# Kernel optimization log

Hardware: AMD Instinct MI355X
Metric: run time of the kernel (lower is better)

Reference implementation:

```python
import jax, jax.numpy as jnp
import numpy as np

ROI = 400
HEADS = 4
DEPTH = 2
RATIO = 0.7
NUM_CLASSES = 2
DH = ROI // HEADS          # dim_head = 100
SCALE = DH ** -0.5
B = 64
HID = 2 * ROI              # ffn hidden = dim * 2


def setup_inputs() -> dict:
    key = jax.random.key(0)
    ks = jax.random.split(key, 24)
    s = 0.02

    def rn(k, shape, scale=s):
        return jax.random.normal(k, shape, dtype=jnp.float32) * scale

    inputs = jax.random.uniform(ks[0], (B, ROI, 2 * ROI), dtype=jnp.float32)
    return {
        "inputs": inputs,
        # structural feature selector (torch init: ones)
        "sc_sel": jnp.ones((ROI, ROI), jnp.float32),
        # attention (per layer, stacked): linears stored [in, out]
        "wq": rn(ks[1], (DEPTH, ROI, ROI)),
        "wk": rn(ks[2], (DEPTH, ROI, ROI)),
        "wv": rn(ks[3], (DEPTH, ROI, ROI)),
        "wo": rn(ks[4], (DEPTH, ROI, ROI)),
        "bo": jnp.zeros((DEPTH, ROI), jnp.float32),
        # feedforward
        "ffn_w1": rn(ks[5], (DEPTH, ROI, HID)),
        "ffn_b1": jnp.zeros((DEPTH, HID), jnp.float32),
        "ffn_w2": rn(ks[6], (DEPTH, HID, ROI)),
        "ffn_b2": jnp.zeros((DEPTH, ROI), jnp.float32),
        "ln_g": jnp.ones((DEPTH, ROI), jnp.float32),
        "ln_b": jnp.zeros((DEPTH, ROI), jnp.float32),
        # pooling (only layer 0's pooling is used since depth=2)
        "pool_ws": rn(ks[7], (ROI, 1), 1.0),
        "pool_wf": rn(ks[8], (ROI, 1), 1.0),
        "pmlp_w": rn(ks[9], (2, 1), 0.5),
        "pmlp_b": jnp.zeros((1,), jnp.float32),
        # readouts
        "r1w": rn(ks[10], (DEPTH, ROI, 128)),
        "r1b": jnp.zeros((DEPTH, 128), jnp.float32),
        "r2w": rn(ks[11], (DEPTH, 128, NUM_CLASSES)),
        "r2b": jnp.zeros((DEPTH, NUM_CLASSES), jnp.float32),
    }


def _layer_norm(x, g, b, eps=1e-5):
    mu = x.mean(-1, keepdims=True)
    var = ((x - mu) ** 2).mean(-1, keepdims=True)
    return (x - mu) * jax.lax.rsqrt(var + eps) * g + b


def _attention(x, m, wq, wk, wv, wo, bo):
    b, n, d = x.shape
    q = (x @ wq).reshape(b, n, HEADS, DH)
    k = (x @ wk).reshape(b, n, HEADS, DH)
    v = (x @ wv).reshape(b, n, HEADS, DH)
    dots = jnp.einsum("bihd,bjhd->bhij", q, k) * SCALE
    dots = dots * (1.0 + m[:, None])        # mask-modulated scores
    attn = jax.nn.softmax(dots, axis=-1)
    out = jnp.einsum("bhij,bjhd->bihd", attn, v).reshape(b, n, HEADS * DH)
    return out @ wo + bo


def _pool(x, m, pool_ws, pool_wf, pmlp_w, pmlp_b):
    b, n, d = x.shape
    k = int(RATIO * n)                       # static under jit
    s1 = jnp.sqrt(jnp.sum((m @ pool_ws[:n]) ** 2, axis=-1))   # [B, N]
    s2 = jnp.sqrt(jnp.sum((x @ pool_wf) ** 2, axis=-1))       # [B, N]
    S = jnp.stack([s1, s2], axis=-1)                          # [B, N, 2]
    scores = jax.nn.sigmoid((S @ pmlp_w + pmlp_b)).squeeze(-1)  # [B, N]
    _, idx = jax.lax.top_k(scores, k)
    idx = jnp.sort(idx, axis=-1)                              # [B, k]
    x_p = jnp.take_along_axis(x, idx[:, :, None], axis=1)     # [B, k, D]
    sw = jnp.take_along_axis(scores, idx, axis=1)[:, :, None]
    x_p = x_p * sw
    m_p = jax.vmap(lambda mb, ib: mb[ib[:, None], ib[None, :]])(m, idx)
    return x_p, m_p


def _forward(inputs, sc_sel, wq, wk, wv, wo, bo, ffn_w1, ffn_b1, ffn_w2,
             ffn_b2, ln_g, ln_b, pool_ws, pool_wf, pmlp_w, pmlp_b,
             r1w, r1b, r2w, r2b):
    fc = inputs[:, :, :ROI]
    sc = inputs[:, :, ROI:]
    sc = jnp.log10(sc + 1.0)
    mean = sc.mean(axis=(1, 2), keepdims=True)
    std = jnp.std(sc, axis=(1, 2), keepdims=True, ddof=1) + 1e-6
    sc = (sc - mean) / std
    M = sc * jax.nn.sigmoid(sc_sel)
    X = fc
    probs = []
    for i in range(DEPTH):
        X = _attention(X, M, wq[i], wk[i], wv[i], wo[i], bo[i]) + X
        h = jax.nn.gelu(X @ ffn_w1[i] + ffn_b1[i], approximate=False)
        h = h @ ffn_w2[i] + ffn_b2[i]
        X = _layer_norm(h + X, ln_g[i], ln_b[i])
        gf = X.mean(axis=1)
        logits = jax.nn.leaky_relu(gf @ r1w[i] + r1b[i], 0.01) @ r2w[i] + r2b[i]
        probs.append(jax.nn.softmax(logits, axis=-1))
        if i < DEPTH - 1:
            X, M = _pool(X, M, pool_ws, pool_wf, pmlp_w, pmlp_b)
    final_prob = jnp.stack(probs, axis=0).mean(axis=0)
    feat = X.mean(axis=1)
    feat = feat / jnp.maximum(jnp.linalg.norm(feat, axis=1, keepdims=True), 1e-12)
    return feat, final_prob


def reference(inputs, sc_sel, wq, wk, wv, wo, bo, ffn_w1, ffn_b1, ffn_w2,
              ffn_b2, ln_g, ln_b, pool_ws, pool_wf, pmlp_w, pmlp_b,
              r1w, r1b, r2w, r2b):
    return _forward(inputs, sc_sel, wq, wk, wv, wo, bo, ffn_w1, ffn_b1,
                    ffn_w2, ffn_b2, ln_g, ln_b, pool_ws, pool_wf, pmlp_w,
                    pmlp_b, r1w, r1b, r2w, r2b)
```

## Files before the change

kernel.cpp:

```cpp
#include <hip/hip_runtime.h>
#include <math.h>

#define ROI 400
#define HEADS 4
#define DH 100
#define NB 64
#define HIDF 800
#define NC 2
#define KPOOL 280
#define ATT_SCALE 0.1f
#define CTT 10

typedef __attribute__((ext_vector_type(8))) short short8v;
typedef __attribute__((ext_vector_type(8))) unsigned short u16x8;
typedef __attribute__((ext_vector_type(4))) float f32x4;

union U8 { short8v v; unsigned short u[8]; };

__device__ __forceinline__ unsigned short f2bf(float x) {
  unsigned int u = __float_as_uint(x);
  u += 0x7fffu + ((u >> 16) & 1u);
  return (unsigned short)(u >> 16);
}
__device__ __forceinline__ void split2(float x, unsigned short& h, unsigned short& l) {
  h = f2bf(x);
  float hf = __uint_as_float(((unsigned int)h) << 16);
  l = f2bf(x - hf);
}

__global__ __launch_bounds__(256) void pre_partial_kernel(const float* __restrict__ in,
                                                          double* __restrict__ pp) {
  int b = blockIdx.x, t = blockIdx.y;
  const float* p = in + (size_t)b * ROI * (2 * ROI);
  float s = 0.f, ss = 0.f;
  for (int e = threadIdx.x; e < 40 * ROI; e += 256) {
    int r = 40 * t + e / ROI, c = e % ROI;
    float v = log10f(p[(size_t)r * (2 * ROI) + ROI + c] + 1.0f);
    s += v; ss += v * v;
  }
  __shared__ double rs[256], rss[256];
  rs[threadIdx.x] = s; rss[threadIdx.x] = ss;
  __syncthreads();
  for (int st = 128; st > 0; st >>= 1) {
    if (threadIdx.x < st) { rs[threadIdx.x] += rs[threadIdx.x + st]; rss[threadIdx.x] += rss[threadIdx.x + st]; }
    __syncthreads();
  }
  if (threadIdx.x == 0) {
    pp[(b * CTT + t) * 2 + 0] = rs[0];
    pp[(b * CTT + t) * 2 + 1] = rss[0];
  }
}

__global__ __launch_bounds__(64) void pre_final_kernel(const double* __restrict__ pp,
                                                       float* __restrict__ meanb,
                                                       float* __restrict__ stdb) {
  int b = threadIdx.x;
  double s = 0.0, ss = 0.0;
  for (int t = 0; t < CTT; ++t) { s += pp[(b * CTT + t) * 2]; ss += pp[(b * CTT + t) * 2 + 1]; }
  const int n = ROI * ROI;
  double mean = s / n;
  double var = (ss - s * s / n) / (double)(n - 1);
  meanb[b] = (float)mean;
  stdb[b]  = (float)(sqrt(var) + 1e-6);
}

__global__ __launch_bounds__(256) void build_m_kernel(const float* __restrict__ in,
                                                      const float* __restrict__ sel,
                                                      const float* __restrict__ meanb,
                                                      const float* __restrict__ stdb,
                                                      float* __restrict__ M) {
  size_t e = (size_t)blockIdx.x * blockDim.x + threadIdx.x;
  const size_t total = (size_t)NB * ROI * ROI;
  if (e >= total) return;
  int c = (int)(e % ROI);
  int r = (int)((e / ROI) % ROI);
  int b = (int)(e / ((size_t)ROI * ROI));
  const float* row = in + ((size_t)b * ROI + r) * (2 * ROI);
  float v = log10f(row[ROI + c] + 1.0f);
  float sg = 1.0f / (1.0f + expf(-sel[r * ROI + c]));
  M[e] = ((v - meanb[b]) / stdb[b]) * sg;
}

struct PackDesc {
  const float* W;
  unsigned short* WH;
  unsigned short* WL;
  int K, N, nbx, blk0;
};
struct PackAll { PackDesc d[6]; };

__global__ __launch_bounds__(256) void packall_kernel(PackAll pa) {
  int gb = blockIdx.x;
  int i = 0;
#pragma unroll
  for (int j = 1; j < 6; ++j) if (gb >= pa.d[j].blk0) i = j;
  const float* __restrict__ W = pa.d[i].W;
  unsigned short* __restrict__ WH = pa.d[i].WH;
  unsigned short* __restrict__ WL = pa.d[i].WL;
  const int K = pa.d[i].K, N = pa.d[i].N;
  int lb = gb - pa.d[i].blk0;
  int bn = (lb % pa.d[i].nbx) * 64;
  int bk = (lb / pa.d[i].nbx) * 64;

  __shared__ float t[64][68];
  int r = threadIdx.x >> 2;
  int c0 = (threadIdx.x & 3) << 4;
  int gk = bk + r;
#pragma unroll
  for (int q = 0; q < 4; ++q) {
    int c = c0 + 4 * q;
    float4 v = make_float4(0.f, 0.f, 0.f, 0.f);
    if (gk < K && bn + c < N) v = *(const float4*)(W + (size_t)gk * N + bn + c);
    *(float4*)&t[r][c] = v;
  }
  __syncthreads();
  int gn = bn + r;
#pragma unroll
  for (int q = 0; q < 4; ++q) {
    int c = c0 + 4 * q;
    int gkk = bk + c;
    if (gn < N && gkk < K) {
      ushort4 h, l;
      split2(t[c + 0][r], h.x, l.x);
      split2(t[c + 1][r], h.y, l.y);
      split2(t[c + 2][r], h.z, l.z);
      split2(t[c + 3][r], h.w, l.w);
      *(ushort4*)(WH + (size_t)gn * K + gkk) = h;
      *(ushort4*)(WL + (size_t)gn * K + gkk) = l;
    }
  }
}

__global__ __launch_bounds__(256) void packa_kernel(const float* __restrict__ A, int lda, int K, int total4,
                                                    unsigned short* __restrict__ AH,
                                                    unsigned short* __restrict__ AL) {
  int e = blockIdx.x * 256 + threadIdx.x;
  if (e >= total4) return;
  int idx = e << 2;
  int row = idx / K, k = idx - row * K;
  float4 v = *(const float4*)(A + (size_t)row * lda + k);
  ushort4 h, l;
  split2(v.x, h.x, l.x); split2(v.y, h.y, l.y);
  split2(v.z, h.z, l.z); split2(v.w, h.w, l.w);
  *(ushort4*)(AH + (size_t)row * K + k) = h;
  *(ushort4*)(AL + (size_t)row * K + k) = l;
}

#define TBM 128
#define TBN 128
#define TBK 32
#define KP 40

template<int EPI>
__global__ __launch_bounds__(256) void mgemm_kernel(const unsigned short* __restrict__ AHp,
                                                    const unsigned short* __restrict__ ALp,
                                                    const unsigned short* __restrict__ WH,
                                                    const unsigned short* __restrict__ WL,
                                                    const float* __restrict__ bias,
                                                    const float* __restrict__ res, int ldr,
                                                    float* __restrict__ C,
                                                    unsigned short* __restrict__ CH,
                                                    unsigned short* __restrict__ CL,
                                                    int M, int N, int K) {
  __shared__ unsigned short Ah[TBM][KP], Al[TBM][KP], Bh[TBN][KP], Bl[TBN][KP];
  const int tid = threadIdx.x;
  const int lane = tid & 63;
  const int wid = tid >> 6;
  const int wm = wid >> 1, wn = wid & 1;
  const int l15 = lane & 15, l4 = lane >> 4;
  const int bm = blockIdx.y * TBM;
  const int bn = blockIdx.x * TBN;

  f32x4 acc[4][4];
#pragma unroll
  for (int i = 0; i < 4; ++i)
#pragma unroll
    for (int j = 0; j < 4; ++j) acc[i][j] = (f32x4){0.f, 0.f, 0.f, 0.f};

  for (int k0 = 0; k0 < K; k0 += TBK) {
#pragma unroll
    for (int it = 0; it < 2; ++it) {
      int c = tid + 256 * it;
      int row = c >> 2;
      int kq = (c & 3) << 3;
      u16x8 vh = {0, 0, 0, 0, 0, 0, 0, 0};
      u16x8 vl = {0, 0, 0, 0, 0, 0, 0, 0};
      if (k0 + kq + 8 <= K) {
        size_t off = (size_t)(bm + row) * K + k0 + kq;
        vh = *(const u16x8*)(AHp + off);
        vl = *(const u16x8*)(ALp + off);
      }
      *(u16x8*)&Ah[row][kq] = vh;
      *(u16x8*)&Al[row][kq] = vl;
    }
#pragma unroll
    for (int it = 0; it < 2; ++it) {
      int c = tid + 256 * it;
      int row = c >> 2;
      int kq = (c & 3) << 3;
      int gn = bn + row;
      u16x8 vh = {0, 0, 0, 0, 0, 0, 0, 0};
      u16x8 vl = {0, 0, 0, 0, 0, 0, 0, 0};
      if (gn < N && k0 + kq + 8 <= K) {
        size_t off = (size_t)gn * K + k0 + kq;
        vh = *(const u16x8*)(WH + off);
        vl = *(const u16x8*)(WL + off);
      }
      *(u16x8*)&Bh[row][kq] = vh;
      *(u16x8*)&Bl[row][kq] = vl;
    }
    __syncthreads();

    short8v ah[4], alo[4], bh[4], blo[4];
#pragma unroll
    for (int mf = 0; mf < 4; ++mf) {
      int r = wm * 64 + mf * 16 + l15;
      ah[mf]  = *(const short8v*)&Ah[r][l4 * 8];
      alo[mf] = *(const short8v*)&Al[r][l4 * 8];
    }
#pragma unroll
    for (int nf = 0; nf < 4; ++nf) {
      int r = wn * 64 + nf * 16 + l15;
      bh[nf]  = *(const short8v*)&Bh[r][l4 * 8];
      blo[nf] = *(const short8v*)&Bl[r][l4 * 8];
    }
#pragma unroll
    for (int mf = 0; mf < 4; ++mf)
#pragma unroll
      for (int nf = 0; nf < 4; ++nf) {
        acc[mf][nf] = __builtin_amdgcn_mfma_f32_16x16x32_bf16(ah[mf], bh[nf], acc[mf][nf], 0, 0, 0);
        acc[mf][nf] = __builtin_amdgcn_mfma_f32_16x16x32_bf16(ah[mf], blo[nf], acc[mf][nf], 0, 0, 0);
        acc[mf][nf] = __builtin_amdgcn_mfma_f32_16x16x32_bf16(alo[mf], bh[nf], acc[mf][nf], 0, 0, 0);
      }
    __syncthreads();
  }

#pragma unroll
  for (int mf = 0; mf < 4; ++mf) {
#pragma unroll
    for (int nf = 0; nf < 4; ++nf) {
      int col = bn + wn * 64 + nf * 16 + l15;
      if (col < N) {
        float bv = (EPI >= 1 && EPI != 6) ? bias[col] : 0.f;
        int row0 = bm + wm * 64 + mf * 16 + l4 * 4;
#pragma unroll
        for (int r = 0; r < 4; ++r) {
          float v = acc[mf][nf][r] + bv;
          int row = row0 + r;
          if (EPI == 2 || EPI == 5) v += res[(size_t)row * ldr + col];
          if (EPI == 4) {
            v = 0.5f * v * (1.0f + erff(v * 0.70710678118654752f));
            unsigned short hh, ll;
            split2(v, hh, ll);
            CH[(size_t)row * N + col] = hh;
            CL[(size_t)row * N + col] = ll;
          } else if (EPI == 5) {
            C[(size_t)row * N + col] = v;
            unsigned short hh, ll;
            split2(v, hh, ll);
            CH[(size_t)row * N + col] = hh;
            CL[(size_t)row * N + col] = ll;
          } else if (EPI == 6) {
            unsigned short hh, ll;
            split2(v, hh, ll);
            CH[(size_t)row * N + col] = hh;
            CL[(size_t)row * N + col] = ll;
          } else {
            C[(size_t)row * N + col] = v;
          }
        }
      }
    }
  }
}

#define FBJ 32

__global__ __launch_bounds__(256) void fattn_kernel(const unsigned short* __restrict__ QKVH,
                                                    const unsigned short* __restrict__ QKVL,
                                                    const float* __restrict__ Mm,
                                                    unsigned short* __restrict__ OH,
                                                    unsigned short* __restrict__ OL, int N) {
  const int ldq = 3 * ROI;
  __shared__ unsigned short Kh[FBJ][136], Kl[FBJ][136];
  __shared__ unsigned short Vth[112][40], Vtl[112][40];
  __shared__ unsigned short Ph[64][40], Pl[64][40];

  const int tid = threadIdx.x;
  const int lane = tid & 63;
  const int w = tid >> 6;
  const int l15 = lane & 15, l4 = lane >> 4;
  const int h = blockIdx.x & (HEADS - 1);
  const int b = blockIdx.x >> 2;
  const int i0 = blockIdx.y * 64;

  const float* Mb = Mm + (size_t)b * N * N;

  for (int e = tid; e < 12 * 40; e += 256) {
    Vth[100 + e / 40][e % 40] = 0; Vtl[100 + e / 40][e % 40] = 0;
  }

  int qr = i0 + 16 * w + l15; if (qr >= N) qr = N - 1;
  const unsigned short* qrH = QKVH + ((size_t)b * N + qr) * ldq + h * DH;
  const unsigned short* qrL = QKVL + ((size_t)b * N + qr) * ldq + h * DH;
  short8v qh[4], ql[4];
#pragma unroll
  for (int kg = 0; kg < 4; ++kg) {
    int d0v = kg * 32 + l4 * 8;
    U8 th, tl;
    if (d0v + 8 <= DH) {
      *(ushort4*)&th.u[0] = *(const ushort4*)(qrH + d0v);
      *(ushort4*)&th.u[4] = *(const ushort4*)(qrH + d0v + 4);
      *(ushort4*)&tl.u[0] = *(const ushort4*)(qrL + d0v);
      *(ushort4*)&tl.u[4] = *(const ushort4*)(qrL + d0v + 4);
    } else if (d0v < DH) {
      *(ushort4*)&th.u[0] = *(const ushort4*)(qrH + d0v);
      *(ushort4*)&tl.u[0] = *(const ushort4*)(qrL + d0v);
#pragma unroll
      for (int j = 4; j < 8; ++j) { th.u[j] = 0; tl.u[j] = 0; }
    } else {
#pragma unroll
      for (int j = 0; j < 8; ++j) { th.u[j] = 0; tl.u[j] = 0; }
    }
    qh[kg] = th.v; ql[kg] = tl.v;
  }

  float m_i[4], l_i[4];
  f32x4 o[7];
#pragma unroll
  for (int r = 0; r < 4; ++r) { m_i[r] = -INFINITY; l_i[r] = 0.f; }
#pragma unroll
  for (int ff = 0; ff < 7; ++ff) o[ff] = (f32x4){0.f, 0.f, 0.f, 0.f};

  const int njt = (N + FBJ - 1) / FBJ;
  for (int jt = 0; jt < njt; ++jt) {
    const int j0 = jt * FBJ;
    const int kv0 = j0 + l15, kv1 = j0 + l15 + 16;

    float mpre[4][2];
#pragma unroll
    for (int r = 0; r < 4; ++r) {
      int gq = i0 + 16 * w + l4 * 4 + r;
      int gqc = (gq < N) ? gq : N - 1;
      const float* Mr = Mb + (size_t)gqc * N;
      mpre[r][0] = (kv0 < N) ? Mr[kv0] : 0.f;
      mpre[r][1] = (kv1 < N) ? Mr[kv1] : 0.f;
    }

    __syncthreads();
    for (int e = tid; e < 32 * 32; e += 256) {
      int kv = e >> 5;
      int dq = (e & 31) << 2;
      int gj = j0 + kv; if (gj >= N) gj = N - 1;
      size_t off = ((size_t)b * N + gj) * ldq + ROI + h * DH + dq;
      ushort4 hh = {0, 0, 0, 0}, ll = {0, 0, 0, 0};
      if (dq < DH) { hh = *(const ushort4*)(QKVH + off); ll = *(const ushort4*)(QKVL + off); }
      *(ushort4*)&Kh[kv][dq] = hh;
      *(ushort4*)&Kl[kv][dq] = ll;
    }
    for (int e = tid; e < 400; e += 256) {
      int kvp = e & 15;
      int dq = (e >> 4) << 2;
      int gj0 = j0 + 2 * kvp;     if (gj0 >= N) gj0 = N - 1;
      int gj1 = j0 + 2 * kvp + 1; if (gj1 >= N) gj1 = N - 1;
      size_t o0 = ((size_t)b * N + gj0) * ldq + 2 * ROI + h * DH + dq;
      size_t o1 = ((size_t)b * N + gj1) * ldq + 2 * ROI + h * DH + dq;
      ushort4 aH = *(const ushort4*)(QKVH + o0);
      ushort4 bH = *(const ushort4*)(QKVH + o1);
      ushort4 aL = *(const ushort4*)(QKVL + o0);
      ushort4 bL = *(const ushort4*)(QKVL + o1);
      *(unsigned int*)&Vth[dq + 0][2 * kvp] = (unsigned int)aH.x | ((unsigned int)bH.x << 16);
      *(unsigned int*)&Vth[dq + 1][2 * kvp] = (unsigned int)aH.y | ((unsigned int)bH.y << 16);
      *(unsigned int*)&Vth[dq + 2][2 * kvp] = (unsigned int)aH.z | ((unsigned int)bH.z << 16);
      *(unsigned int*)&Vth[dq + 3][2 * kvp] = (unsigned int)aH.w | ((unsigned int)bH.w << 16);
      *(unsigned int*)&Vtl[dq + 0][2 * kvp] = (unsigned int)aL.x | ((unsigned int)bL.x << 16);
      *(unsigned int*)&Vtl[dq + 1][2 * kvp] = (unsigned int)aL.y | ((unsigned int)bL.y << 16);
      *(unsigned int*)&Vtl[dq + 2][2 * kvp] = (unsigned int)aL.z | ((unsigned int)bL.z << 16);
      *(unsigned int*)&Vtl[dq + 3][2 * kvp] = (unsigned int)aL.w | ((unsigned int)bL.w << 16);
    }
    __syncthreads();

    f32x4 sacc[2];
    sacc[0] = (f32x4){0.f, 0.f, 0.f, 0.f};
    sacc[1] = (f32x4){0.f, 0.f, 0.f, 0.f};
#pragma unroll
    for (int kg = 0; kg < 4; ++kg) {
#pragma unroll
      for (int f = 0; f < 2; ++f) {
        short8v bh = *(const short8v*)&Kh[l15 + 16 * f][kg * 32 + l4 * 8];
        short8v bl = *(const short8v*)&Kl[l15 + 16 * f][kg * 32 + l4 * 8];
        sacc[f] = __builtin_amdgcn_mfma_f32_16x16x32_bf16(qh[kg], bh, sacc[f], 0, 0, 0);
        sacc[f] = __builtin_amdgcn_mfma_f32_16x16x32_bf16(qh[kg], bl, sacc[f], 0, 0, 0);
        sacc[f] = __builtin_amdgcn_mfma_f32_16x16x32_bf16(ql[kg], bh, sacc[f], 0, 0, 0);
      }
    }

#pragma unroll
    for (int r = 0; r < 4; ++r) {
      float s0 = (kv0 < N) ? sacc[0][r] * ATT_SCALE * (1.0f + mpre[r][0]) : -INFINITY;
      float s1 = (kv1 < N) ? sacc[1][r] * ATT_SCALE * (1.0f + mpre[r][1]) : -INFINITY;
      float rm = fmaxf(s0, s1);
      rm = fmaxf(rm, __shfl_xor(rm, 1, 16));
      rm = fmaxf(rm, __shfl_xor(rm, 2, 16));
      rm = fmaxf(rm, __shfl_xor(rm, 4, 16));
      rm = fmaxf(rm, __shfl_xor(rm, 8, 16));
      float nm = fmaxf(m_i[r], rm);
      float fr = expf(m_i[r] - nm);
      float p0 = (kv0 < N) ? expf(s0 - nm) : 0.f;
      float p1 = (kv1 < N) ? expf(s1 - nm) : 0.f;
      float ts = p0 + p1;
      ts += __shfl_xor(ts, 1, 16);
      ts += __shfl_xor(ts, 2, 16);
      ts += __shfl_xor(ts, 4, 16);
      ts += __shfl_xor(ts, 8, 16);
      l_i[r] = l_i[r] * fr + ts;
      m_i[r] = nm;
#pragma unroll
      for (int ff = 0; ff < 7; ++ff) o[ff][r] *= fr;
      unsigned short h0, l0, h1, l1;
      split2(p0, h0, l0); split2(p1, h1, l1);
      int prow = 16 * w + l4 * 4 + r;
      Ph[prow][l15] = h0;      Pl[prow][l15] = l0;
      Ph[prow][l15 + 16] = h1; Pl[prow][l15 + 16] = l1;
    }
    __syncthreads();

    short8v ph = *(const short8v*)&Ph[16 * w + l15][l4 * 8];
    short8v pl = *(const short8v*)&Pl[16 * w + l15][l4 * 8];
#pragma unroll
    for (int ff = 0; ff < 7; ++ff) {
      short8v vh = *(const short8v*)&Vth[ff * 16 + l15][l4 * 8];
      short8v vl = *(const short8v*)&Vtl[ff * 16 + l15][l4 * 8];
      o[ff] = __builtin_amdgcn_mfma_f32_16x16x32_bf16(ph, vh, o[ff], 0, 0, 0);
      o[ff] = __builtin_amdgcn_mfma_f32_16x16x32_bf16(ph, vl, o[ff], 0, 0, 0);
      o[ff] = __builtin_amdgcn_mfma_f32_16x16x32_bf16(pl, vh, o[ff], 0, 0, 0);
    }
  }

#pragma unroll
  for (int r = 0; r < 4; ++r) {
    int gq = i0 + 16 * w + l4 * 4 + r;
    if (gq < N) {
      float inv = 1.0f / l_i[r];
      size_t rowoff = ((size_t)b * N + gq) * ROI + h * DH;
#pragma unroll
      for (int ff = 0; ff < 7; ++ff) {
        int d = ff * 16 + l15;
        if (d < DH) {
          unsigned short hh, ll;
          split2(o[ff][r] * inv, hh, ll);
          OH[rowoff + d] = hh;
          OL[rowoff + d] = ll;
        }
      }
    }
  }
}

__global__ __launch_bounds__(128) void ln_kernel(const float* __restrict__ Y, const float* __restrict__ g,
                                                 const float* __restrict__ bta, float* __restrict__ X) {
  int row = blockIdx.x;
  const float* y = Y + (size_t)row * ROI;
  float* x = X + (size_t)row * ROI;
  int tid = threadIdx.x;
  __shared__ float red[128];
  float s = 0.f;
  for (int c = tid; c < ROI; c += 128) s += y[c];
  red[tid] = s; __syncthreads();
  for (int st = 64; st > 0; st >>= 1) { if (tid < st) red[tid] += red[tid + st]; __syncthreads(); }
  float mu = red[0] / ROI;
  __syncthreads();
  float v = 0.f;
  for (int c = tid; c < ROI; c += 128) { float d = y[c] - mu; v += d * d; }
  red[tid] = v; __syncthreads();
  for (int st = 64; st > 0; st >>= 1) { if (tid < st) red[tid] += red[tid + st]; __syncthreads(); }
  float rstd = rsqrtf(red[0] / ROI + 1e-5f);
  for (int c = tid; c < ROI; c += 128) x[c] = (y[c] - mu) * rstd * g[c] + bta[c];
}

__global__ __launch_bounds__(128) void colmean_kernel(const float* __restrict__ X,
                                                      float* __restrict__ gfp, int N) {
  int b = blockIdx.x, t = blockIdx.y, tid = threadIdx.x;
  int per = (N + CTT - 1) / CTT;
  int n0 = t * per, n1 = n0 + per;
  if (n1 > N) n1 = N;
  float a0 = 0.f, a1 = 0.f, a2 = 0.f, a3 = 0.f;
  for (int n = n0; n < n1; ++n) {
    const float* row = X + ((size_t)b * N + n) * ROI;
    a0 += row[tid]; a1 += row[tid + 128]; a2 += row[tid + 256];
    if (tid < 16) a3 += row[tid + 384];
  }
  float* g = gfp + ((size_t)b * CTT + t) * ROI;
  g[tid] = a0; g[tid + 128] = a1; g[tid + 256] = a2;
  if (tid < 16) g[tid + 384] = a3;
}

__global__ __launch_bounds__(128) void head_kernel(const float* __restrict__ gfp,
                                                   const float* __restrict__ r1w, const float* __restrict__ r1b,
                                                   const float* __restrict__ r2w, const float* __restrict__ r2b,
                                                   float* __restrict__ probs, int N) {
  int b = blockIdx.x, tid = threadIdx.x;
  __shared__ float gf[ROI];
  __shared__ float hid[128];
  for (int c = tid; c < ROI; c += 128) {
    float s = 0.f;
    for (int t = 0; t < CTT; ++t) s += gfp[((size_t)b * CTT + t) * ROI + c];
    gf[c] = s / (float)N;
  }
  __syncthreads();
  {
    float a = r1b[tid];
    for (int k = 0; k < ROI; ++k) a += gf[k] * r1w[k * 128 + tid];
    hid[tid] = (a >= 0.f) ? a : 0.01f * a;
  }
  __syncthreads();
  if (tid < NC) {
    float l = r2b[tid];
    for (int k = 0; k < 128; ++k) l += hid[k] * r2w[k * NC + tid];
    gf[tid] = l;
  }
  __syncthreads();
  if (tid == 0) {
    float m = fmaxf(gf[0], gf[1]);
    float e0 = expf(gf[0] - m), e1 = expf(gf[1] - m);
    float inv = 1.f / (e0 + e1);
    probs[b * NC + 0] = e0 * inv;
    probs[b * NC + 1] = e1 * inv;
  }
}

__global__ __launch_bounds__(128) void finalize_kernel(const float* __restrict__ gfp,
                                                       const float* __restrict__ probs,
                                                       float* __restrict__ out, int N) {
  int b = blockIdx.x, tid = threadIdx.x;
  __shared__ float f[ROI];
  __shared__ float red[128];
  for (int c = tid; c < ROI; c += 128) {
    float s = 0.f;
    for (int t = 0; t < CTT; ++t) s += gfp[((size_t)b * CTT + t) * ROI + c];
    f[c] = s / (float)N;
  }
  __syncthreads();
  float ls = 0.f;
  for (int c = tid; c < ROI; c += 128) ls += f[c] * f[c];
  red[tid] = ls; __syncthreads();
  for (int st = 64; st > 0; st >>= 1) { if (tid < st) red[tid] += red[tid + st]; __syncthreads(); }
  float inv = 1.f / fmaxf(sqrtf(red[0]), 1e-12f);
  for (int c = tid; c < ROI; c += 128) out[b * ROI + c] = f[c] * inv;
  if (tid < NC) out[NB * ROI + b * NC + tid] = 0.5f * (probs[b * NC + tid] + probs[NB * NC + b * NC + tid]);
}

__global__ __launch_bounds__(128) void score_kernel(const float* __restrict__ M, const float* __restrict__ X,
                                                    const float* __restrict__ pws, const float* __restrict__ pwf,
                                                    const float* __restrict__ pmw, const float* __restrict__ pmb,
                                                    float* __restrict__ scores) {
  int i = blockIdx.x, b = blockIdx.y, tid = threadIdx.x;
  const float* mr = M + ((size_t)b * ROI + i) * ROI;
  const float* xr = X + ((size_t)b * ROI + i) * ROI;
  float s1 = 0.f, s2 = 0.f;
  for (int j = tid; j < ROI; j += 128) { s1 += mr[j] * pws[j]; s2 += xr[j] * pwf[j]; }
  __shared__ float r1[128], r2[128];
  r1[tid] = s1; r2[tid] = s2; __syncthreads();
  for (int st = 64; st > 0; st >>= 1) {
    if (tid < st) { r1[tid] += r1[tid + st]; r2[tid] += r2[tid + st]; }
    __syncthreads();
  }
  if (tid == 0) {
    float a = fabsf(r1[0]), c = fabsf(r2[0]);
    float z = a * pmw[0] + c * pmw[1] + pmb[0];
    scores[b * ROI + i] = 1.f / (1.f + expf(-z));
  }
}

__global__ __launch_bounds__(128) void select_kernel(const float* __restrict__ scores, int* __restrict__ idx) {
  int b = blockIdx.x, tid = threadIdx.x;
  __shared__ float sc[ROI];
  __shared__ int sel[ROI];
  for (int i = tid; i < ROI; i += 128) sc[i] = scores[b * ROI + i];
  __syncthreads();
  for (int i = tid; i < ROI; i += 128) {
    float si = sc[i];
    int rank = 0;
    for (int j = 0; j < ROI; ++j) {
      float sj = sc[j];
      rank += (sj > si) || (sj == si && j < i);
    }
    sel[i] = (rank < KPOOL) ? 1 : 0;
  }
  __syncthreads();
  for (int i = tid; i < ROI; i += 128) {
    if (sel[i]) {
      int pos = 0;
      for (int j = 0; j < i; ++j) pos += sel[j];
      idx[b * KPOOL + pos] = i;
    }
  }
}

__global__ __launch_bounds__(128) void gatherx_kernel(const float* __restrict__ X, const float* __restrict__ scores,
                                                      const int* __restrict__ idx, float* __restrict__ Xp,
                                                      unsigned short* __restrict__ XpH,
                                                      unsigned short* __restrict__ XpL) {
  int p = blockIdx.x % KPOOL, b = blockIdx.x / KPOOL, tid = threadIdx.x;
  int src = idx[b * KPOOL + p];
  float sw = scores[b * ROI + src];
  const float* xr = X + ((size_t)b * ROI + src) * ROI;
  size_t ro = ((size_t)b * KPOOL + p) * ROI;
  float* o = Xp + ro;
  for (int c = tid; c < ROI; c += 128) {
    float v = xr[c] * sw;
    o[c] = v;
    unsigned short hh, ll;
    split2(v, hh, ll);
    XpH[ro + c] = hh;
    XpL[ro + c] = ll;
  }
}

__global__ __launch_bounds__(128) void gatherm_kernel(const float* __restrict__ M, const int* __restrict__ idx,
                                                      float* __restrict__ Mp) {
  int p = blockIdx.x % KPOOL, b = blockIdx.x / KPOOL, tid = threadIdx.x;
  __shared__ int id[KPOOL];
  for (int q = tid; q < KPOOL; q += 128) id[q] = idx[b * KPOOL + q];
  __syncthreads();
  int src = idx[b * KPOOL + p];
  const float* mr = M + ((size_t)b * ROI + src) * ROI;
  float* o = Mp + ((size_t)b * KPOOL + p) * KPOOL;
  for (int q = tid; q < KPOOL; q += 128) o[q] = mr[id[q]];
}

template<int EPI>
static inline void mgemm(const unsigned short* AH, const unsigned short* AL,
                         const unsigned short* WH, const unsigned short* WL,
                         const float* bias, const float* res, int ldr,
                         float* C, unsigned short* CH, unsigned short* CL,
                         int M, int N, int K, hipStream_t st) {
  dim3 g((N + TBN - 1) / TBN, M / TBM);
  mgemm_kernel<EPI><<<g, 256, 0, st>>>(AH, AL, WH, WL, bias, res, ldr, C, CH, CL, M, N, K);
}

static inline void packa(const float* A, int lda, int M, int K, unsigned short* AH, unsigned short* AL,
                         hipStream_t st) {
  int total4 = M * K / 4;
  packa_kernel<<<(total4 + 255) / 256, 256, 0, st>>>(A, lda, K, total4, AH, AL);
}

static inline void pack_depth(const float* wq, const float* wk, const float* wv, const float* wo,
                              const float* w1, const float* w2,
                              unsigned short* qkvH, unsigned short* qkvL,
                              unsigned short* woH, unsigned short* woL,
                              unsigned short* w1H, unsigned short* w1L,
                              unsigned short* w2H, unsigned short* w2L, hipStream_t st) {
  PackAll pa;
  int blk = 0;
  auto add = [&](int i, const float* W, unsigned short* WH, unsigned short* WL, int K, int N) {
    int nbx = (N + 63) / 64, nby = (K + 63) / 64;
    pa.d[i] = {W, WH, WL, K, N, nbx, blk};
    blk += nbx * nby;
  };
  add(0, wq, qkvH + 0,      qkvL + 0,      ROI, ROI);
  add(1, wk, qkvH + 160000, qkvL + 160000, ROI, ROI);
  add(2, wv, qkvH + 320000, qkvL + 320000, ROI, ROI);
  add(3, wo, woH, woL, ROI, ROI);
  add(4, w1, w1H, w1L, ROI, HIDF);
  add(5, w2, w2H, w2L, HIDF, ROI);
  packall_kernel<<<blk, 256, 0, st>>>(pa);
}

extern "C" void kernel_launch(void* const* d_in, const int* in_sizes, int n_in,
                              void* d_out, int out_size, void* d_ws, size_t ws_size,
                              hipStream_t stream) {
  const float* in  = (const float*)d_in[0];
  const float* sel = (const float*)d_in[1];
  const float* wq  = (const float*)d_in[2];
  const float* wk  = (const float*)d_in[3];
  const float* wv  = (const float*)d_in[4];
  const float* wo  = (const float*)d_in[5];
  const float* bo  = (const float*)d_in[6];
  const float* w1  = (const float*)d_in[7];
  const float* b1  = (const float*)d_in[8];
  const float* w2  = (const float*)d_in[9];
  const float* b2  = (const float*)d_in[10];
  const float* lng = (const float*)d_in[11];
  const float* lnb = (const float*)d_in[12];
  const float* pws = (const float*)d_in[13];
  const float* pwf = (const float*)d_in[14];
  const float* pmw = (const float*)d_in[15];
  const float* pmb = (const float*)d_in[16];
  const float* r1w = (const float*)d_in[17];
  const float* r1b = (const float*)d_in[18];
  const float* r2w = (const float*)d_in[19];
  const float* r2b = (const float*)d_in[20];
  float* out = (float*)d_out;

  float* ws = (float*)d_ws;
  const size_t AT = (size_t)NB * ROI * ROI;

  unsigned short* up = (unsigned short*)ws;
  unsigned short* qkvH = up;
  unsigned short* qkvL = up + 480000;
  unsigned short* woH  = up + 960000;
  unsigned short* woL  = up + 1120000;
  unsigned short* w1H  = up + 1280000;
  unsigned short* w1L  = up + 1600000;
  unsigned short* w2H  = up + 1920000;
  unsigned short* w2L  = up + 2240000;

  float* smalls = ws + 6 * AT;
  float* meanb = smalls;
  float* stdb  = smalls + 64;
  float* scores = smalls + 128;
  int*   idx = (int*)(smalls + 128 + NB * ROI);
  float* probs = smalls + 128 + NB * ROI + NB * KPOOL;
  double* pp = (double*)(smalls + 128 + NB * ROI + NB * KPOOL + 2 * NB * NC + 16);

  float* Mmask = ws + AT;

  pre_partial_kernel<<<dim3(NB, CTT), 256, 0, stream>>>(in, pp);
  pre_final_kernel<<<1, 64, 0, stream>>>(pp, meanb, stdb);
  build_m_kernel<<<(int)((AT + 255) / 256), 256, 0, stream>>>(in, sel, meanb, stdb, Mmask);

  {
    const int N = ROI;
    const int Mtok = NB * N;
    pack_depth(wq, wk, wv, wo, w1, w2, qkvH, qkvL, woH, woL, w1H, w1L, w2H, w2L, stream);

    unsigned short* AinH = (unsigned short*)(ws + 5 * AT);
    unsigned short* AinL = AinH + (size_t)Mtok * ROI;
    packa(in, 2 * ROI, Mtok, ROI, AinH, AinL, stream);

    unsigned short* QKVH_ = (unsigned short*)(ws + 2 * AT);
    unsigned short* QKVL_ = QKVH_ + (size_t)Mtok * (3 * ROI);
    mgemm<6>(AinH, AinL, qkvH, qkvL, nullptr, nullptr, 0, nullptr, QKVH_, QKVL_,
             Mtok, 3 * ROI, ROI, stream);

    unsigned short* OpH = (unsigned short*)(ws + 5 * AT);
    unsigned short* OpL = OpH + (size_t)Mtok * ROI;
    fattn_kernel<<<dim3(NB * HEADS, (N + 63) / 64), 256, 0, stream>>>(
        QKVH_, QKVL_, Mmask, OpH, OpL, N);

    float* Xa0 = ws + 2 * AT;
    unsigned short* XaH = (unsigned short*)(ws + 3 * AT);
    unsigned short* XaL = XaH + (size_t)Mtok * ROI;
    mgemm<5>(OpH, OpL, woH, woL, bo, in, 2 * ROI, Xa0, XaH, XaL,
             Mtok, ROI, ROI, stream);

    unsigned short* Hh = (unsigned short*)(ws + 4 * AT);
    unsigned short* Hl = (unsigned short*)(ws + 5 * AT);
    mgemm<4>(XaH, XaL, w1H, w1L, b1, nullptr, 0, nullptr, Hh, Hl,
             Mtok, HIDF, ROI, stream);

    float* Y0 = ws + 3 * AT;
    mgemm<2>(Hh, Hl, w2H, w2L, b2, Xa0, ROI, Y0, nullptr, nullptr,
             Mtok, ROI, HIDF, stream);

    float* Xn = ws + 2 * AT;
    ln_kernel<<<Mtok, 128, 0, stream>>>(Y0, lng, lnb, Xn);

    float* gfp0 = ws + 3 * AT;
    colmean_kernel<<<dim3(NB, CTT), 128, 0, stream>>>(Xn, gfp0, N);
    head_kernel<<<NB, 128, 0, stream>>>(gfp0, r1w, r1b, r2w, r2b, probs, N);

    score_kernel<<<dim3(ROI, NB), 128, 0, stream>>>(Mmask, Xn, pws, pwf, pmw, pmb, scores);
    select_kernel<<<NB, 128, 0, stream>>>(scores, idx);
    float* Mp = ws + 4 * AT + 1200000;
    gatherm_kernel<<<NB * KPOOL, 128, 0, stream>>>(Mmask, idx, Mp);
    float* Xp = ws + 5 * AT;
    unsigned short* XpH = (unsigned short*)(ws + AT);
    unsigned short* XpL = XpH + (size_t)NB * KPOOL * ROI;
    gatherx_kernel<<<NB * KPOOL, 128, 0, stream>>>(Xn, scores, idx, Xp, XpH, XpL);
  }

  {
    const int N = KPOOL;
    const int Mtok = NB * N;
    const int d = 1;
    const float* wq1 = wq + (size_t)d * ROI * ROI;
    const float* wk1 = wk + (size_t)d * ROI * ROI;
    const float* wv1 = wv + (size_t)d * ROI * ROI;
    const float* wo1 = wo + (size_t)d * ROI * ROI;
    const float* bo1 = bo + (size_t)d * ROI;
    const float* w11 = w1 + (size_t)d * ROI * HIDF;
    const float* b11 = b1 + (size_t)d * HIDF;
    const float* w21 = w2 + (size_t)d * HIDF * ROI;
    const float* b21 = b2 + (size_t)d * ROI;
    const float* lng1 = lng + (size_t)d * ROI;
    const float* lnb1 = lnb + (size_t)d * ROI;
    const float* r1w1 = r1w + (size_t)d * ROI * 128;
    const float* r1b1 = r1b + (size_t)d * 128;
    const float* r2w1 = r2w + (size_t)d * 128 * NC;
    const float* r2b1 = r2b + (size_t)d * NC;

    float* Xp = ws + 5 * AT;
    float* Mp = ws + 4 * AT + 1200000;
    unsigned short* XpH = (unsigned short*)(ws + AT);
    unsigned short* XpL = XpH + (size_t)Mtok * ROI;

    pack_depth(wq1, wk1, wv1, wo1, w11, w21, qkvH, qkvL, woH, woL, w1H, w1L, w2H, w2L, stream);

    unsigned short* QKVH_ = (unsigned short*)(ws + 2 * AT);
    unsigned short* QKVL_ = QKVH_ + (size_t)Mtok * (3 * ROI);
    mgemm<6>(XpH, XpL, qkvH, qkvL, nullptr, nullptr, 0, nullptr, QKVH_, QKVL_,
             Mtok, 3 * ROI, ROI, stream);

    unsigned short* OpH = (unsigned short*)(ws + AT);
    unsigned short* OpL = OpH + (size_t)Mtok * ROI;
    fattn_kernel<<<dim3(NB * HEADS, (N + 63) / 64), 256, 0, stream>>>(
        QKVH_, QKVL_, Mp, OpH, OpL, N);

    float* Xa1 = ws + 2 * AT;
    unsigned short* XaH = (unsigned short*)(ws + 3 * AT);
    unsigned short* XaL = XaH + (size_t)Mtok * ROI;
    mgemm<5>(OpH, OpL, woH, woL, bo1, Xp, ROI, Xa1, XaH, XaL,
             Mtok, ROI, ROI, stream);

    unsigned short* H1h = (unsigned short*)(ws + 4 * AT);
    unsigned short* H1l = (unsigned short*)(ws + 5 * AT);
    mgemm<4>(XaH, XaL, w1H, w1L, b11, nullptr, 0, nullptr, H1h, H1l,
             Mtok, HIDF, ROI, stream);

    float* Y1 = ws + AT;
    mgemm<2>(H1h, H1l, w2H, w2L, b21, Xa1, ROI, Y1, nullptr, nullptr,
             Mtok, ROI, HIDF, stream);

    float* Xf = ws + 3 * AT;
    ln_kernel<<<Mtok, 128, 0, stream>>>(Y1, lng1, lnb1, Xf);

    float* gfp1 = ws + 2 * AT;
    colmean_kernel<<<dim3(NB, CTT), 128, 0, stream>>>(Xf, gfp1, N);
    head_kernel<<<NB, 128, 0, stream>>>(gfp1, r1w1, r1b1, r2w1, r2b1, probs + NB * NC, N);
    finalize_kernel<<<NB, 128, 0, stream>>>(gfp1, probs, out, N);
  }
  (void)in_sizes; (void)n_in; (void)out_size; (void)ws_size;
}
```

Baseline: 1.574 ms.

## Register-prefetch next K/V/mask tile in flash attention and raise MFMA priority

The flash-attention kernel now loads the next tile's K, V and mask values into registers while the current tile's MFMAs run, then writes them to shared memory after the next barrier. This hides global-load latency that previously sat on the critical path between barriers. It also wraps the MFMA sections in s_setprio and reorders the block index so consecutive blocks share a head across different batches. The cost is higher register pressure, which could reduce occupancy.

```diff
diff --git a/kernel.cpp b/kernel.cpp
--- a/kernel.cpp
+++ b/kernel.cpp
@@ -290,8 +290,8 @@
   const int lane = tid & 63;
   const int w = tid >> 6;
   const int l15 = lane & 15, l4 = lane >> 4;
-  const int h = blockIdx.x & (HEADS - 1);
-  const int b = blockIdx.x >> 2;
+  const int b = blockIdx.x & (NB - 1);
+  const int h = blockIdx.x >> 6;
   const int i0 = blockIdx.y * 64;
 
   const float* Mb = Mm + (size_t)b * N * N;
@@ -325,6 +325,52 @@
     qh[kg] = th.v; ql[kg] = tl.v;
   }
 
+  ushort4 kHp[4], kLp[4];
+  ushort4 vAH[2], vBH[2], vAL[2], vBL[2];
+  float mnext[4][2];
+
+  {
+    const int j0 = 0;
+#pragma unroll
+    for (int it = 0; it < 4; ++it) {
+      int e = tid + 256 * it;
+      int kv = e >> 5, dq = (e & 31) << 2;
+      int gj = j0 + kv; if (gj >= N) gj = N - 1;
+      ushort4 hh = {0, 0, 0, 0}, ll = {0, 0, 0, 0};
+      if (dq < DH) {
+        size_t off = ((size_t)b * N + gj) * ldq + ROI + h * DH + dq;
+        hh = *(const ushort4*)(QKVH + off); ll = *(const ushort4*)(QKVL + off);
+      }
+      kHp[it] = hh; kLp[it] = ll;
+    }
+#pragma unroll
+    for (int it = 0; it < 2; ++it) {
+      int e = tid + 256 * it;
+      ushort4 z = {0, 0, 0, 0};
+      vAH[it] = z; vBH[it] = z; vAL[it] = z; vBL[it] = z;
+      if (e < 400) {
+        int kvp = e & 15, dq = (e >> 4) << 2;
+        int gj0 = j0 + 2 * kvp;     if (gj0 >= N) gj0 = N - 1;
+        int gj1 = j0 + 2 * kvp + 1; if (gj1 >= N) gj1 = N - 1;
+        size_t o0 = ((size_t)b * N + gj0) * ldq + 2 * ROI + h * DH + dq;
+        size_t o1 = ((size_t)b * N + gj1) * ldq + 2 * ROI + h * DH + dq;
+        vAH[it] = *(const ushort4*)(QKVH + o0);
+        vBH[it] = *(const ushort4*)(QKVH + o1);
+        vAL[it] = *(const ushort4*)(QKVL + o0);
+        vBL[it] = *(const ushort4*)(QKVL + o1);
+      }
+    }
+#pragma unroll
+    for (int r = 0; r < 4; ++r) {
+      int gq = i0 + 16 * w + l4 * 4 + r;
+      int gqc = (gq < N) ? gq : N - 1;
+      const float* Mr = Mb + (size_t)gqc * N;
+      int kv0 = j0 + l15, kv1 = j0 + l15 + 16;
+      mnext[r][0] = (kv0 < N) ? Mr[kv0] : 0.f;
+      mnext[r][1] = (kv1 < N) ? Mr[kv1] : 0.f;
+    }
+  }
+
   float m_i[4], l_i[4];
   f32x4 o[7];
 #pragma unroll
@@ -337,52 +383,78 @@
     const int j0 = jt * FBJ;
     const int kv0 = j0 + l15, kv1 = j0 + l15 + 16;
 
-    float mpre[4][2];
-#pragma unroll
-    for (int r = 0; r < 4; ++r) {
-      int gq = i0 + 16 * w + l4 * 4 + r;
-      int gqc = (gq < N) ? gq : N - 1;
-      const float* Mr = Mb + (size_t)gqc * N;
-      mpre[r][0] = (kv0 < N) ? Mr[kv0] : 0.f;
-      mpre[r][1] = (kv1 < N) ? Mr[kv1] : 0.f;
-    }
-
     __syncthreads();
-    for (int e = tid; e < 32 * 32; e += 256) {
-      int kv = e >> 5;
-      int dq = (e & 31) << 2;
-      int gj = j0 + kv; if (gj >= N) gj = N - 1;
-      size_t off = ((size_t)b * N + gj) * ldq + ROI + h * DH + dq;
-      ushort4 hh = {0, 0, 0, 0}, ll = {0, 0, 0, 0};
-      if (dq < DH) { hh = *(const ushort4*)(QKVH + off); ll = *(const ushort4*)(QKVL + off); }
-      *(ushort4*)&Kh[kv][dq] = hh;
-      *(ushort4*)&Kl[kv][dq] = ll;
-    }
-    for (int e = tid; e < 400; e += 256) {
-      int kvp = e & 15;
-      int dq = (e >> 4) << 2;
-      int gj0 = j0 + 2 * kvp;     if (gj0 >= N) gj0 = N - 1;
-      int gj1 = j0 + 2 * kvp + 1; if (gj1 >= N) gj1 = N - 1;
-      size_t o0 = ((size_t)b * N + gj0) * ldq + 2 * ROI + h * DH + dq;
-      size_t o1 = ((size_t)b * N + gj1) * ldq + 2 * ROI + h * DH + dq;
-      ushort4 aH = *(const ushort4*)(QKVH + o0);
-      ushort4 bH = *(const ushort4*)(QKVH + o1);
-      ushort4 aL = *(const ushort4*)(QKVL + o0);
-      ushort4 bL = *(const ushort4*)(QKVL + o1);
-      *(unsigned int*)&Vth[dq + 0][2 * kvp] = (unsigned int)aH.x | ((unsigned int)bH.x << 16);
-      *(unsigned int*)&Vth[dq + 1][2 * kvp] = (unsigned int)aH.y | ((unsigned int)bH.y << 16);
-      *(unsigned int*)&Vth[dq + 2][2 * kvp] = (unsigned int)aH.z | ((unsigned int)bH.z << 16);
-      *(unsigned int*)&Vth[dq + 3][2 * kvp] = (unsigned int)aH.w | ((unsigned int)bH.w << 16);
-      *(unsigned int*)&Vtl[dq + 0][2 * kvp] = (unsigned int)aL.x | ((unsigned int)bL.x << 16);
-      *(unsigned int*)&Vtl[dq + 1][2 * kvp] = (unsigned int)aL.y | ((unsigned int)bL.y << 16);
-      *(unsigned int*)&Vtl[dq + 2][2 * kvp] = (unsigned int)aL.z | ((unsigned int)bL.z << 16);
-      *(unsigned int*)&Vtl[dq + 3][2 * kvp] = (unsigned int)aL.w | ((unsigned int)bL.w << 16);
-    }
+#pragma unroll
+    for (int it = 0; it < 4; ++it) {
+      int e = tid + 256 * it;
+      int kv = e >> 5, dq = (e & 31) << 2;
+      *(ushort4*)&Kh[kv][dq] = kHp[it];
+      *(ushort4*)&Kl[kv][dq] = kLp[it];
+    }
+#pragma unroll
+    for (int it = 0; it < 2; ++it) {
+      int e = tid + 256 * it;
+      if (e < 400) {
+        int kvp = e & 15, dq = (e >> 4) << 2;
+        *(unsigned int*)&Vth[dq + 0][2 * kvp] = (unsigned int)vAH[it].x | ((unsigned int)vBH[it].x << 16);
+        *(unsigned int*)&Vth[dq + 1][2 * kvp] = (unsigned int)vAH[it].y | ((unsigned int)vBH[it].y << 16);
+        *(unsigned int*)&Vth[dq + 2][2 * kvp] = (unsigned int)vAH[it].z | ((unsigned int)vBH[it].z << 16);
+        *(unsigned int*)&Vth[dq + 3][2 * kvp] = (unsigned int)vAH[it].w | ((unsigned int)vBH[it].w << 16);
+        *(unsigned int*)&Vtl[dq + 0][2 * kvp] = (unsigned int)vAL[it].x | ((unsigned int)vBL[it].x << 16);
+        *(unsigned int*)&Vtl[dq + 1][2 * kvp] = (unsigned int)vAL[it].y | ((unsigned int)vBL[it].y << 16);
+        *(unsigned int*)&Vtl[dq + 2][2 * kvp] = (unsigned int)vAL[it].z | ((unsigned int)vBL[it].z << 16);
+        *(unsigned int*)&Vtl[dq + 3][2 * kvp] = (unsigned int)vAL[it].w | ((unsigned int)vBL[it].w << 16);
+      }
+    }
+    float mcur[4][2];
+#pragma unroll
+    for (int r = 0; r < 4; ++r) { mcur[r][0] = mnext[r][0]; mcur[r][1] = mnext[r][1]; }
     __syncthreads();
+
+    if (jt + 1 < njt) {
+      const int jn = j0 + FBJ;
+#pragma unroll
+      for (int it = 0; it < 4; ++it) {
+        int e = tid + 256 * it;
+        int kv = e >> 5, dq = (e & 31) << 2;
+        int gj = jn + kv; if (gj >= N) gj = N - 1;
+        ushort4 hh = {0, 0, 0, 0}, ll = {0, 0, 0, 0};
+        if (dq < DH) {
+          size_t off = ((size_t)b * N + gj) * ldq + ROI + h * DH + dq;
+          hh = *(const ushort4*)(QKVH + off); ll = *(const ushort4*)(QKVL + off);
+        }
+        kHp[it] = hh; kLp[it] = ll;
+      }
+#pragma unroll
+      for (int it = 0; it < 2; ++it) {
+        int e = tid + 256 * it;
+        if (e < 400) {
+          int kvp = e & 15, dq = (e >> 4) << 2;
+          int gj0 = jn + 2 * kvp;     if (gj0 >= N) gj0 = N - 1;
+          int gj1 = jn + 2 * kvp + 1; if (gj1 >= N) gj1 = N - 1;
+          size_t o0 = ((size_t)b * N + gj0) * ldq + 2 * ROI + h * DH + dq;
+          size_t o1 = ((size_t)b * N + gj1) * ldq + 2 * ROI + h * DH + dq;
+          vAH[it] = *(const ushort4*)(QKVH + o0);
+          vBH[it] = *(const ushort4*)(QKVH + o1);
+          vAL[it] = *(const ushort4*)(QKVL + o0);
+          vBL[it] = *(const ushort4*)(QKVL + o1);
+        }
+      }
+#pragma unroll
+      for (int r = 0; r < 4; ++r) {
+        int gq = i0 + 16 * w + l4 * 4 + r;
+        int gqc = (gq < N) ? gq : N - 1;
+        const float* Mr = Mb + (size_t)gqc * N;
+        int nkv0 = jn + l15, nkv1 = jn + l15 + 16;
+        mnext[r][0] = (nkv0 < N) ? Mr[nkv0] : 0.f;
+        mnext[r][1] = (nkv1 < N) ? Mr[nkv1] : 0.f;
+      }
+    }
 
     f32x4 sacc[2];
     sacc[0] = (f32x4){0.f, 0.f, 0.f, 0.f};
     sacc[1] = (f32x4){0.f, 0.f, 0.f, 0.f};
+    __builtin_amdgcn_s_setprio(1);
 #pragma unroll
     for (int kg = 0; kg < 4; ++kg) {
 #pragma unroll
@@ -394,11 +466,12 @@
         sacc[f] = __builtin_amdgcn_mfma_f32_16x16x32_bf16(ql[kg], bh, sacc[f], 0, 0, 0);
       }
     }
+    __builtin_amdgcn_s_setprio(0);
 
 #pragma unroll
     for (int r = 0; r < 4; ++r) {
-      float s0 = (kv0 < N) ? sacc[0][r] * ATT_SCALE * (1.0f + mpre[r][0]) : -INFINITY;
-      float s1 = (kv1 < N) ? sacc[1][r] * ATT_SCALE * (1.0f + mpre[r][1]) : -INFINITY;
+      float s0 = (kv0 < N) ? sacc[0][r] * ATT_SCALE * (1.0f + mcur[r][0]) : -INFINITY;
+      float s1 = (kv1 < N) ? sacc[1][r] * ATT_SCALE * (1.0f + mcur[r][1]) : -INFINITY;
       float rm = fmaxf(s0, s1);
       rm = fmaxf(rm, __shfl_xor(rm, 1, 16));
       rm = fmaxf(rm, __shfl_xor(rm, 2, 16));
@@ -427,6 +500,7 @@
 
     short8v ph = *(const short8v*)&Ph[16 * w + l15][l4 * 8];
     short8v pl = *(const short8v*)&Pl[16 * w + l15][l4 * 8];
+    __builtin_amdgcn_s_setprio(1);
 #pragma unroll
     for (int ff = 0; ff < 7; ++ff) {
       short8v vh = *(const short8v*)&Vth[ff * 16 + l15][l4 * 8];
@@ -435,6 +509,7 @@
       o[ff] = __builtin_amdgcn_mfma_f32_16x16x32_bf16(ph, vl, o[ff], 0, 0, 0);
       o[ff] = __builtin_amdgcn_mfma_f32_16x16x32_bf16(pl, vh, o[ff], 0, 0, 0);
     }
+    __builtin_amdgcn_s_setprio(0);
   }
 
 #pragma unroll
@@ -736,7 +811,7 @@
 
     unsigned short* OpH = (unsigned short*)(ws + 5 * AT);
     unsigned short* OpL = OpH + (size_t)Mtok * ROI;
-    fattn_kernel<<<dim3(NB * HEADS, (N + 63) / 64), 256, 0, stream>>>(
+    fattn_kernel<<<dim3(HEADS * NB, (N + 63) / 64), 256, 0, stream>>>(
         QKVH_, QKVL_, Mmask, OpH, OpL, N);
 
     float* Xa0 = ws + 2 * AT;
@@ -805,7 +880,7 @@
 
     unsigned short* OpH = (unsigned short*)(ws + AT);
     unsigned short* OpL = OpH + (size_t)Mtok * ROI;
-    fattn_kernel<<<dim3(NB * HEADS, (N + 63) / 64), 256, 0, stream>>>(
+    fattn_kernel<<<dim3(HEADS * NB, (N + 63) / 64), 256, 0, stream>>>(
         QKVH_, QKVL_, Mp, OpH, OpL, N);
 
     float* Xa1 = ws + 2 * AT;
```

Measured after the change: 1.442 ms. 8.4% less time.
